# Performance work log

Hardware: AMD Instinct MI355X
Metric: run time of the kernel (lower is better)

## Reference

```python
import jax, jax.numpy as jnp
import numpy as np

EMBED = 1024
HEADS = 16
HEAD_DIM = EMBED // HEADS
B, L = 4, 2048


def setup_inputs() -> dict:
    key = jax.random.key(0)
    ks = jax.random.split(key, 10)
    s = 1.0 / np.sqrt(EMBED)
    x = jax.random.normal(ks[0], (B, L, EMBED), dtype=jnp.float32)
    mask = jax.random.randint(ks[1], (B, 1, L, L), 0, 2, dtype=jnp.int32)
    Wq = jax.random.normal(ks[2], (EMBED, EMBED), dtype=jnp.float32) * s
    Wk = jax.random.normal(ks[3], (EMBED, EMBED), dtype=jnp.float32) * s
    Wv = jax.random.normal(ks[4], (EMBED, EMBED), dtype=jnp.float32) * s
    Wo = jax.random.normal(ks[5], (EMBED, EMBED), dtype=jnp.float32) * s
    bq = jnp.zeros((EMBED,), jnp.float32)
    bk = jnp.zeros((EMBED,), jnp.float32)
    bv = jnp.zeros((EMBED,), jnp.float32)
    bo = jnp.zeros((EMBED,), jnp.float32)
    return {"x": x, "mask": mask, "Wq": Wq, "bq": bq, "Wk": Wk, "bk": bk,
            "Wv": Wv, "bv": bv, "Wo": Wo, "bo": bo}


def reference(x, mask, Wq, bq, Wk, bk, Wv, bv, Wo, bo):
    n, l, _ = x.shape
    q = (x @ Wq + bq).reshape(n, l, HEADS, HEAD_DIM)
    k = (x @ Wk + bk).reshape(n, l, HEADS, HEAD_DIM)
    v = (x @ Wv + bv).reshape(n, l, HEADS, HEAD_DIM)
    # [n, h, q, k] scores
    energy = jnp.einsum('nqhd,nkhd->nhqk', q, k)
    energy = jnp.where(mask == 0, jnp.float32(-1e20), energy)
    attn = jax.nn.softmax(energy / jnp.sqrt(jnp.float32(HEAD_DIM)), axis=-1)
    out = jnp.einsum('nhqk,nkhd->nqhd', attn, v).reshape(n, l, EMBED)
    return out @ Wo + bo
```

## Files before the change

kernel.cpp:

```cpp
#include <hip/hip_runtime.h>
#include <hip/hip_bf16.h>

#define EMBED 1024
#define HEADS 16
#define HDIM 64
#define BATCH 4
#define SEQ 2048
#define ROWS (BATCH * SEQ)
#define LOG2E 1.4426950408889634f

typedef __attribute__((ext_vector_type(8))) short bf16x8;
typedef __attribute__((ext_vector_type(4))) float f32x4;

#define MFMA16(a, b, c) __builtin_amdgcn_mfma_f32_16x16x32_bf16(a, b, c, 0, 0, 0)

__device__ __forceinline__ unsigned short f2bf(float f) {
    union { float f; unsigned int u; } x; x.f = f;
    unsigned int r = x.u + 0x7fffu + ((x.u >> 16) & 1u);
    return (unsigned short)(r >> 16);
}

__device__ __forceinline__ unsigned int pkbf(float a, float b) {
#if __has_builtin(__builtin_amdgcn_cvt_pk_bf16_f32)
    auto v = __builtin_amdgcn_cvt_pk_bf16_f32(a, b);
    unsigned int u; __builtin_memcpy(&u, &v, 4); return u;
#else
    union { __hip_bfloat162 h; unsigned int u; } c;
    c.h = __float22bfloat162_rn(make_float2(a, b)); return c.u;
#endif
}

__device__ __forceinline__ void gl2lds(const unsigned short* g, unsigned short* l) {
    __builtin_amdgcn_global_load_lds(
        (const __attribute__((address_space(1))) unsigned int*)g,
        (__attribute__((address_space(3))) unsigned int*)l, 16, 0, 0);
}

#define XBLK 8192
#define MBLK 16384
#define WBLK 4096

__global__ __launch_bounds__(256) void prep_kernel(
    const float* __restrict__ x, const int* __restrict__ mask,
    const float* __restrict__ W0, const float* __restrict__ W1,
    const float* __restrict__ W2, const float* __restrict__ W3,
    unsigned short* __restrict__ Xb, unsigned char* __restrict__ m8,
    unsigned short* __restrict__ Wt)
{
    __shared__ float t[32][33];
    const int bid = blockIdx.x;
    if (bid < XBLK) {
        int i = (bid * 256 + threadIdx.x) * 4;
        float4 v = *(const float4*)(x + i);
        uint2 o; o.x = pkbf(v.x, v.y); o.y = pkbf(v.z, v.w);
        *(uint2*)(Xb + i) = o;
    } else if (bid < XBLK + MBLK) {
        int i = ((bid - XBLK) * 256 + threadIdx.x) * 4;
        int4 v = *(const int4*)(mask + i);
        uchar4 o;
        o.x = v.x ? 0xFF : 0; o.y = v.y ? 0xFF : 0;
        o.z = v.z ? 0xFF : 0; o.w = v.w ? 0xFF : 0;
        *(uchar4*)(m8 + i) = o;
    } else {
        int f = bid - XBLK - MBLK;
        int z = f >> 10, rem = f & 1023;
        const float* W = (z == 0) ? W0 : (z == 1) ? W1 : (z == 2) ? W2 : W3;
        unsigned short* o = Wt + (size_t)z * EMBED * EMBED;
        int tx = threadIdx.x & 31, ty = threadIdx.x >> 5;
        int bx = (rem & 31) * 32, by = (rem >> 5) * 32;
#pragma unroll
        for (int r = 0; r < 32; r += 8)
            t[ty + r][tx] = W[(size_t)(by + ty + r) * EMBED + bx + tx];
        __syncthreads();
#pragma unroll
        for (int r = 0; r < 32; r += 8)
            o[(size_t)(bx + ty + r) * EMBED + by + tx] = f2bf(t[tx][ty + r]);
    }
}

__device__ __forceinline__ void gemm_bf16_body(
    const unsigned short* __restrict__ A, const unsigned short* __restrict__ Bt,
    const float* __restrict__ bias,
    float* __restrict__ outF, unsigned short* __restrict__ outB, float scale,
    int vmode)
{
    __shared__ unsigned short As[128][64];
    __shared__ unsigned short Bs[128][64];
    const int tid = threadIdx.x;
    const int lane = tid & 63, wid = tid >> 6;
    const int ln = lane & 15, lg = lane >> 4;
    const int wy = wid >> 1, wx = wid & 1;
    const int m0 = blockIdx.y * 128, n0 = blockIdx.x * 128;
    const int r0 = wid * 32 + (lane >> 3);
    const int scol = (((lane & 7) ^ ((lane >> 3) & 7)) << 3);
    const unsigned short* Ap = A + (size_t)(m0 + r0) * EMBED + scol;
    const unsigned short* Bp = Bt + (size_t)(n0 + r0) * EMBED + scol;
    unsigned short* lA = &As[wid * 32][0];
    unsigned short* lB = &Bs[wid * 32][0];

    f32x4 acc[4][4];
#pragma unroll
    for (int i = 0; i < 4; i++)
#pragma unroll
        for (int j = 0; j < 4; j++) acc[i][j] = (f32x4){0.f, 0.f, 0.f, 0.f};

    for (int k0 = 0; k0 < EMBED; k0 += 64) {
        __syncthreads();
#pragma unroll
        for (int is = 0; is < 4; is++) {
            gl2lds(Ap + k0 + (size_t)(is * 8) * EMBED, lA + is * 8 * 64);
            gl2lds(Bp + k0 + (size_t)(is * 8) * EMBED, lB + is * 8 * 64);
        }
        __syncthreads();
        bf16x8 af[2][4], bfr[2][4];
#pragma unroll
        for (int s = 0; s < 2; s++) {
#pragma unroll
            for (int mi = 0; mi < 4; mi++)
                af[s][mi] = *(const bf16x8*)
                    &As[wy * 64 + mi * 16 + ln][(((lg + 4 * s) ^ (ln & 7)) << 3)];
#pragma unroll
            for (int nj = 0; nj < 4; nj++)
                bfr[s][nj] = *(const bf16x8*)
                    &Bs[wx * 64 + nj * 16 + ln][(((lg + 4 * s) ^ (ln & 7)) << 3)];
        }
#pragma unroll
        for (int s = 0; s < 2; s++)
#pragma unroll
            for (int mi = 0; mi < 4; mi++)
#pragma unroll
                for (int nj = 0; nj < 4; nj++)
                    acc[mi][nj] = MFMA16(af[s][mi], bfr[s][nj], acc[mi][nj]);
    }

#pragma unroll
    for (int mi = 0; mi < 4; mi++) {
#pragma unroll
        for (int nj = 0; nj < 4; nj++) {
            int row = m0 + wy * 64 + mi * 16 + lg * 4;
            int col = n0 + wx * 64 + nj * 16 + ln;
            float bv = bias[col];
            if (vmode) {
                int bb = row >> 11, s = row & (SEQ - 1);
                int hh = col >> 6, dd = col & 63;
                unsigned short* dst = outB +
                    ((size_t)((bb * HEADS + hh) * HDIM + dd)) * SEQ + s;
                uint2 pw;
                pw.x = pkbf(acc[mi][nj][0] + bv, acc[mi][nj][1] + bv);
                pw.y = pkbf(acc[mi][nj][2] + bv, acc[mi][nj][3] + bv);
                *(uint2*)dst = pw;
            } else {
#pragma unroll
                for (int r = 0; r < 4; r++) {
                    float v = (acc[mi][nj][r] + bv) * scale;
                    if (outF) outF[(size_t)(row + r) * EMBED + col] = v;
                    else      outB[(size_t)(row + r) * EMBED + col] = f2bf(v);
                }
            }
        }
    }
}

__global__ __launch_bounds__(256) void qkv_gemm_kernel(
    const unsigned short* __restrict__ Xb, const unsigned short* __restrict__ Wt,
    const float* __restrict__ bq, const float* __restrict__ bk,
    const float* __restrict__ bv,
    unsigned short* __restrict__ Qb, unsigned short* __restrict__ Kb,
    unsigned short* __restrict__ Vt)
{
    int z = blockIdx.z;
    const unsigned short* Bt = Wt + (size_t)z * EMBED * EMBED;
    const float* bias = (z == 0) ? bq : (z == 1) ? bk : bv;
    unsigned short* out = (z == 0) ? Qb : (z == 1) ? Kb : Vt;
    float scale = (z == 0) ? 0.125f * LOG2E : 1.0f;
    gemm_bf16_body(Xb, Bt, bias, nullptr, out, scale, z == 2);
}

__global__ __launch_bounds__(256) void out_gemm_kernel(
    const unsigned short* __restrict__ Ob, const unsigned short* __restrict__ Wto,
    const float* __restrict__ bo, float* __restrict__ out)
{
    gemm_bf16_body(Ob, Wto, bo, out, nullptr, 1.0f, 0);
}

__global__ __launch_bounds__(256) void attn_mfma_kernel(
    const unsigned short* __restrict__ Qb, const unsigned short* __restrict__ Kb,
    const unsigned short* __restrict__ Vt, const unsigned char* __restrict__ mask8,
    unsigned short* __restrict__ Ob)
{
    __shared__ unsigned short Ks[64][64];
    __shared__ unsigned short Vs[64][64];
    __shared__ unsigned short Ps[4][32][64];
    const int tid = threadIdx.x;
    const int lane = tid & 63, wid = tid >> 6;
    const int ln = lane & 15, lg = lane >> 4;
    const int b = blockIdx.z, h = blockIdx.y;
    const int q0 = blockIdx.x * 128 + wid * 32;

    bf16x8 qf[2][2];
#pragma unroll
    for (int mi = 0; mi < 2; mi++)
#pragma unroll
        for (int ks = 0; ks < 2; ks++)
            qf[mi][ks] = *(const bf16x8*)(Qb +
                (size_t)(b * SEQ + q0 + mi * 16 + ln) * EMBED + h * HDIM + ks * 32 + lg * 8);

    bf16x8 ones;
#pragma unroll
    for (int i = 0; i < 8; i++) ones[i] = (short)0x3F80;

    f32x4 o[2][4];
#pragma unroll
    for (int mi = 0; mi < 2; mi++)
#pragma unroll
        for (int dj = 0; dj < 4; dj++) o[mi][dj] = (f32x4){0.f, 0.f, 0.f, 0.f};
    f32x4 lacc[2] = {(f32x4){0.f, 0.f, 0.f, 0.f}, (f32x4){0.f, 0.f, 0.f, 0.f}};

    const int srow = tid >> 3;
    const int scolKV = (((tid & 7) ^ ((tid >> 3) & 7)) << 3);
    const unsigned short* Kp = Kb + (size_t)(b * SEQ + srow) * EMBED + h * HDIM + scolKV;
    const unsigned short* Vp = Vt + (size_t)((b * HEADS + h) * HDIM + srow) * SEQ + scolKV;
    unsigned short* lK = &Ks[srow & ~7][0];
    unsigned short* lV = &Vs[srow & ~7][0];

    const unsigned char* mq0 = mask8 + (size_t)b * SEQ * SEQ + (size_t)(q0 + ln) * SEQ;
    const unsigned char* mq1 = mq0 + (size_t)16 * SEQ;

    const int swk = ((lg ^ (ln & 7)) << 3);

    int pwr[4], prd[2];
#pragma unroll
    for (int nj = 0; nj < 4; nj++)
        pwr[nj] = (((2 * nj + (lg >> 1)) ^ (ln & 7)) << 3) + ((lg & 1) << 2);
#pragma unroll
    for (int ks = 0; ks < 2; ks++)
        prd[ks] = ((4 * ks + lg) ^ (ln & 7)) << 3;
    unsigned short* ps0 = &Ps[wid][ln][0];
    unsigned short* ps1 = &Ps[wid][16 + ln][0];

    for (int kt = 0; kt < SEQ; kt += 64) {
        unsigned int mw[2][4];
#pragma unroll
        for (int mi = 0; mi < 2; mi++) {
            const unsigned char* mq = (mi ? mq1 : mq0) + kt;
#pragma unroll
            for (int nj = 0; nj < 4; nj++)
                mw[mi][nj] = *(const unsigned int*)(mq + nj * 16 + lg * 4);
        }

        __syncthreads();
        gl2lds(Kp + (size_t)kt * EMBED, lK);
        gl2lds(Kp + (size_t)(kt + 32) * EMBED, lK + 32 * 64);
        gl2lds(Vp + kt, lV);
        gl2lds(Vp + (size_t)32 * SEQ + kt, lV + 32 * 64);
        __syncthreads();

        f32x4 S[2][4];
#pragma unroll
        for (int nj = 0; nj < 4; nj++) {
            bf16x8 k0 = *(const bf16x8*)&Ks[nj * 16 + ln][swk];
            bf16x8 k1 = *(const bf16x8*)&Ks[nj * 16 + ln][swk ^ 32];
#pragma unroll
            for (int mi = 0; mi < 2; mi++) {
                f32x4 t2 = (f32x4){0.f, 0.f, 0.f, 0.f};
                t2 = MFMA16(k0, qf[mi][0], t2);
                t2 = MFMA16(k1, qf[mi][1], t2);
                S[mi][nj] = t2;
            }
        }

#pragma unroll
        for (int mi = 0; mi < 2; mi++) {
            unsigned short* psb = mi ? ps1 : ps0;
#pragma unroll
            for (int nj = 0; nj < 4; nj++) {
                float p0 = __builtin_amdgcn_exp2f(S[mi][nj][0]);
                float p1 = __builtin_amdgcn_exp2f(S[mi][nj][1]);
                float p2 = __builtin_amdgcn_exp2f(S[mi][nj][2]);
                float p3 = __builtin_amdgcn_exp2f(S[mi][nj][3]);
                unsigned int m = mw[mi][nj];
                unsigned int d0 = __builtin_amdgcn_perm(0u, m, 0x01010000u);
                unsigned int d1 = __builtin_amdgcn_perm(0u, m, 0x03030202u);
                uint2 pw;
                pw.x = pkbf(p0, p1) & d0;
                pw.y = pkbf(p2, p3) & d1;
                *(uint2*)(psb + pwr[nj]) = pw;
            }
        }

#pragma unroll
        for (int ks = 0; ks < 2; ks++) {
            bf16x8 p0 = *(const bf16x8*)(ps0 + prd[ks]);
            bf16x8 p1 = *(const bf16x8*)(ps1 + prd[ks]);
            lacc[0] = MFMA16(p0, ones, lacc[0]);
            lacc[1] = MFMA16(p1, ones, lacc[1]);
#pragma unroll
            for (int dj = 0; dj < 4; dj++) {
                bf16x8 vf = *(const bf16x8*)&Vs[dj * 16 + ln][swk ^ (ks << 5)];
                o[0][dj] = MFMA16(p0, vf, o[0][dj]);
                o[1][dj] = MFMA16(p1, vf, o[1][dj]);
            }
        }
    }

#pragma unroll
    for (int mi = 0; mi < 2; mi++) {
        float l0 = 1.0f / lacc[mi][0];
        float l1 = 1.0f / lacc[mi][1];
        float l2 = 1.0f / lacc[mi][2];
        float l3 = 1.0f / lacc[mi][3];
#pragma unroll
        for (int dj = 0; dj < 4; dj++) {
            unsigned short* op = Ob + (size_t)(b * SEQ + q0 + mi * 16 + lg * 4) * EMBED
                                    + h * HDIM + dj * 16 + ln;
            op[0]         = f2bf(o[mi][dj][0] * l0);
            op[EMBED]     = f2bf(o[mi][dj][1] * l1);
            op[2 * EMBED] = f2bf(o[mi][dj][2] * l2);
            op[3 * EMBED] = f2bf(o[mi][dj][3] * l3);
        }
    }
}

extern "C" void kernel_launch(void* const* d_in, const int* in_sizes, int n_in,
                              void* d_out, int out_size, void* d_ws, size_t ws_size,
                              hipStream_t stream)
{
    const float* x  = (const float*)d_in[0];
    const int* mask = (const int*)d_in[1];
    const float* Wq = (const float*)d_in[2];
    const float* bq = (const float*)d_in[3];
    const float* Wk = (const float*)d_in[4];
    const float* bk = (const float*)d_in[5];
    const float* Wv = (const float*)d_in[6];
    const float* bv = (const float*)d_in[7];
    const float* Wo = (const float*)d_in[8];
    const float* bo = (const float*)d_in[9];
    float* outp = (float*)d_out;

    char* ws = (char*)d_ws;
    unsigned short* Wt = (unsigned short*)(ws);
    unsigned char*  m8 = (unsigned char*)(ws + ((size_t)8 << 20));
    unsigned short* Xb = (unsigned short*)(ws + ((size_t)24 << 20));
    unsigned short* Ob = Xb;
    unsigned short* Qb = (unsigned short*)(ws + ((size_t)40 << 20));
    unsigned short* Kb = (unsigned short*)(ws + ((size_t)56 << 20));
    unsigned short* Vt = (unsigned short*)(ws + ((size_t)72 << 20));

    prep_kernel<<<XBLK + MBLK + WBLK, 256, 0, stream>>>(
        x, mask, Wq, Wk, Wv, Wo, Xb, m8, Wt);
    qkv_gemm_kernel<<<dim3(EMBED / 128, ROWS / 128, 3), 256, 0, stream>>>(
        Xb, Wt, bq, bk, bv, Qb, Kb, Vt);
    attn_mfma_kernel<<<dim3(SEQ / 128, HEADS, BATCH), 256, 0, stream>>>(
        Qb, Kb, Vt, m8, Ob);
    out_gemm_kernel<<<dim3(EMBED / 128, ROWS / 128), 256, 0, stream>>>(
        Ob, Wt + (size_t)3 * EMBED * EMBED, bo, outp);
}
```

Measured before the change: 403.7 us.

## Prefetch next K/V tile into registers during attention compute

Replaces the synchronous per-iteration global-to-LDS copy of K/V tiles with a register prefetch of the next tile, issued before the current tile's MFMA work and written to LDS afterwards. This is meant to hide global load latency behind the QK and PV matrix math. It also raises wave priority around the MFMA sections and sets a minimum-blocks hint in the launch bounds, which may constrain registers and cause spills given the extra prefetch registers.

```diff
diff --git a/kernel.cpp b/kernel.cpp
--- a/kernel.cpp
+++ b/kernel.cpp
@@ -183,7 +183,7 @@
     gemm_bf16_body(Ob, Wto, bo, out, nullptr, 1.0f, 0);
 }
 
-__global__ __launch_bounds__(256) void attn_mfma_kernel(
+__global__ __launch_bounds__(256, 4) void attn_mfma_kernel(
     const unsigned short* __restrict__ Qb, const unsigned short* __restrict__ Kb,
     const unsigned short* __restrict__ Vt, const unsigned char* __restrict__ mask8,
     unsigned short* __restrict__ Ob)
@@ -223,6 +223,14 @@
     unsigned short* lK = &Ks[srow & ~7][0];
     unsigned short* lV = &Vs[srow & ~7][0];
 
+    gl2lds(Kp, lK);
+    gl2lds(Kp + (size_t)32 * EMBED, lK + 32 * 64);
+    gl2lds(Vp, lV);
+    gl2lds(Vp + (size_t)32 * SEQ, lV + 32 * 64);
+
+    unsigned short* wK = lK + lane * 8;
+    unsigned short* wV = lV + lane * 8;
+
     const unsigned char* mq0 = mask8 + (size_t)b * SEQ * SEQ + (size_t)(q0 + ln) * SEQ;
     const unsigned char* mq1 = mq0 + (size_t)16 * SEQ;
 
@@ -238,6 +246,8 @@
     unsigned short* ps0 = &Ps[wid][ln][0];
     unsigned short* ps1 = &Ps[wid][16 + ln][0];
 
+    __syncthreads();
+
     for (int kt = 0; kt < SEQ; kt += 64) {
         unsigned int mw[2][4];
 #pragma unroll
@@ -248,14 +258,17 @@
                 mw[mi][nj] = *(const unsigned int*)(mq + nj * 16 + lg * 4);
         }
 
-        __syncthreads();
-        gl2lds(Kp + (size_t)kt * EMBED, lK);
-        gl2lds(Kp + (size_t)(kt + 32) * EMBED, lK + 32 * 64);
-        gl2lds(Vp + kt, lV);
-        gl2lds(Vp + (size_t)32 * SEQ + kt, lV + 32 * 64);
-        __syncthreads();
+        uint4 nk0, nk1, nv0, nv1;
+        const int ktn = kt + 64;
+        if (ktn < SEQ) {
+            nk0 = *(const uint4*)(Kp + (size_t)ktn * EMBED);
+            nk1 = *(const uint4*)(Kp + (size_t)(ktn + 32) * EMBED);
+            nv0 = *(const uint4*)(Vp + ktn);
+            nv1 = *(const uint4*)(Vp + (size_t)32 * SEQ + ktn);
+        }
 
         f32x4 S[2][4];
+        __builtin_amdgcn_s_setprio(1);
 #pragma unroll
         for (int nj = 0; nj < 4; nj++) {
             bf16x8 k0 = *(const bf16x8*)&Ks[nj * 16 + ln][swk];
@@ -268,6 +281,7 @@
                 S[mi][nj] = t2;
             }
         }
+        __builtin_amdgcn_s_setprio(0);
 
 #pragma unroll
         for (int mi = 0; mi < 2; mi++) {
@@ -288,6 +302,7 @@
             }
         }
 
+        __builtin_amdgcn_s_setprio(1);
 #pragma unroll
         for (int ks = 0; ks < 2; ks++) {
             bf16x8 p0 = *(const bf16x8*)(ps0 + prd[ks]);
@@ -300,6 +315,16 @@
                 o[0][dj] = MFMA16(p0, vf, o[0][dj]);
                 o[1][dj] = MFMA16(p1, vf, o[1][dj]);
             }
+        }
+        __builtin_amdgcn_s_setprio(0);
+
+        if (ktn < SEQ) {
+            __syncthreads();
+            *(uint4*)wK = nk0;
+            *(uint4*)(wK + 32 * 64) = nk1;
+            *(uint4*)wV = nv0;
+            *(uint4*)(wV + 32 * 64) = nv1;
+            __syncthreads();
         }
     }
 
```

Result: slower. 463.2 us (+14.7%).

## Double-buffer K/V tiles with 32-key steps in attention kernel

Applied to the files above, without the earlier changes.

Shrinks the attention key tile from 64 to 32 and double-buffers the K and V tiles in LDS. The next tile's global-to-LDS load is issued before computing on the current one, so each iteration needs one barrier instead of two. MFMA sections are wrapped with s_setprio to favour matrix issue. The price is twice as many loop iterations and barriers, plus new swizzle indexing for the narrower V and P tiles.

```diff
diff --git a/kernel.cpp b/kernel.cpp
--- a/kernel.cpp
+++ b/kernel.cpp
@@ -188,9 +188,9 @@
     const unsigned short* __restrict__ Vt, const unsigned char* __restrict__ mask8,
     unsigned short* __restrict__ Ob)
 {
-    __shared__ unsigned short Ks[64][64];
-    __shared__ unsigned short Vs[64][64];
-    __shared__ unsigned short Ps[4][32][64];
+    __shared__ unsigned short Ks[2][32][64];
+    __shared__ unsigned short Vs[2][64][32];
+    __shared__ unsigned short Ps[4][32][32];
     const int tid = threadIdx.x;
     const int lane = tid & 63, wid = tid >> 6;
     const int ln = lane & 15, lg = lane >> 4;
@@ -217,49 +217,56 @@
     f32x4 lacc[2] = {(f32x4){0.f, 0.f, 0.f, 0.f}, (f32x4){0.f, 0.f, 0.f, 0.f}};
 
     const int srow = tid >> 3;
-    const int scolKV = (((tid & 7) ^ ((tid >> 3) & 7)) << 3);
-    const unsigned short* Kp = Kb + (size_t)(b * SEQ + srow) * EMBED + h * HDIM + scolKV;
-    const unsigned short* Vp = Vt + (size_t)((b * HEADS + h) * HDIM + srow) * SEQ + scolKV;
-    unsigned short* lK = &Ks[srow & ~7][0];
-    unsigned short* lV = &Vs[srow & ~7][0];
+    const int scolK = (((tid & 7) ^ ((tid >> 3) & 7)) << 3);
+    const int vrow = tid >> 2;
+    const int scolV = (((tid & 3) ^ ((tid >> 2) & 3)) << 3);
+    const unsigned short* Kp = Kb + (size_t)(b * SEQ + srow) * EMBED + h * HDIM + scolK;
+    const unsigned short* Vp = Vt + (size_t)((b * HEADS + h) * HDIM + vrow) * SEQ + scolV;
+
+    gl2lds(Kp, &Ks[0][wid * 8][0]);
+    gl2lds(Vp, &Vs[0][wid * 16][0]);
 
     const unsigned char* mq0 = mask8 + (size_t)b * SEQ * SEQ + (size_t)(q0 + ln) * SEQ;
     const unsigned char* mq1 = mq0 + (size_t)16 * SEQ;
 
     const int swk = ((lg ^ (ln & 7)) << 3);
-
-    int pwr[4], prd[2];
-#pragma unroll
-    for (int nj = 0; nj < 4; nj++)
-        pwr[nj] = (((2 * nj + (lg >> 1)) ^ (ln & 7)) << 3) + ((lg & 1) << 2);
-#pragma unroll
-    for (int ks = 0; ks < 2; ks++)
-        prd[ks] = ((4 * ks + lg) ^ (ln & 7)) << 3;
+    const int vswk = ((lg ^ (ln & 3)) << 3);
+
+    int pwr[2];
+#pragma unroll
+    for (int nj = 0; nj < 2; nj++)
+        pwr[nj] = (((2 * nj + (lg >> 1)) ^ (ln & 3)) << 3) + ((lg & 1) << 2);
+    const int prd = ((lg ^ (ln & 3)) << 3);
     unsigned short* ps0 = &Ps[wid][ln][0];
     unsigned short* ps1 = &Ps[wid][16 + ln][0];
 
-    for (int kt = 0; kt < SEQ; kt += 64) {
-        unsigned int mw[2][4];
+    __syncthreads();
+
+    for (int kt = 0; kt < SEQ; kt += 32) {
+        const int cur = (kt >> 5) & 1;
+
+        unsigned int mw[2][2];
 #pragma unroll
         for (int mi = 0; mi < 2; mi++) {
             const unsigned char* mq = (mi ? mq1 : mq0) + kt;
 #pragma unroll
-            for (int nj = 0; nj < 4; nj++)
+            for (int nj = 0; nj < 2; nj++)
                 mw[mi][nj] = *(const unsigned int*)(mq + nj * 16 + lg * 4);
         }
-
-        __syncthreads();
-        gl2lds(Kp + (size_t)kt * EMBED, lK);
-        gl2lds(Kp + (size_t)(kt + 32) * EMBED, lK + 32 * 64);
-        gl2lds(Vp + kt, lV);
-        gl2lds(Vp + (size_t)32 * SEQ + kt, lV + 32 * 64);
-        __syncthreads();
-
-        f32x4 S[2][4];
-#pragma unroll
-        for (int nj = 0; nj < 4; nj++) {
-            bf16x8 k0 = *(const bf16x8*)&Ks[nj * 16 + ln][swk];
-            bf16x8 k1 = *(const bf16x8*)&Ks[nj * 16 + ln][swk ^ 32];
+        __builtin_amdgcn_sched_barrier(0);
+
+        if (kt + 32 < SEQ) {
+            gl2lds(Kp + (size_t)(kt + 32) * EMBED, &Ks[cur ^ 1][wid * 8][0]);
+            gl2lds(Vp + (kt + 32), &Vs[cur ^ 1][wid * 16][0]);
+        }
+        __builtin_amdgcn_sched_barrier(0);
+
+        f32x4 S[2][2];
+        __builtin_amdgcn_s_setprio(1);
+#pragma unroll
+        for (int nj = 0; nj < 2; nj++) {
+            bf16x8 k0 = *(const bf16x8*)&Ks[cur][nj * 16 + ln][swk];
+            bf16x8 k1 = *(const bf16x8*)&Ks[cur][nj * 16 + ln][swk ^ 32];
 #pragma unroll
             for (int mi = 0; mi < 2; mi++) {
                 f32x4 t2 = (f32x4){0.f, 0.f, 0.f, 0.f};
@@ -268,12 +275,13 @@
                 S[mi][nj] = t2;
             }
         }
+        __builtin_amdgcn_s_setprio(0);
 
 #pragma unroll
         for (int mi = 0; mi < 2; mi++) {
             unsigned short* psb = mi ? ps1 : ps0;
 #pragma unroll
-            for (int nj = 0; nj < 4; nj++) {
+            for (int nj = 0; nj < 2; nj++) {
                 float p0 = __builtin_amdgcn_exp2f(S[mi][nj][0]);
                 float p1 = __builtin_amdgcn_exp2f(S[mi][nj][1]);
                 float p2 = __builtin_amdgcn_exp2f(S[mi][nj][2]);
@@ -288,19 +296,22 @@
             }
         }
 
-#pragma unroll
-        for (int ks = 0; ks < 2; ks++) {
-            bf16x8 p0 = *(const bf16x8*)(ps0 + prd[ks]);
-            bf16x8 p1 = *(const bf16x8*)(ps1 + prd[ks]);
+        __builtin_amdgcn_s_setprio(1);
+        {
+            bf16x8 p0 = *(const bf16x8*)(ps0 + prd);
+            bf16x8 p1 = *(const bf16x8*)(ps1 + prd);
             lacc[0] = MFMA16(p0, ones, lacc[0]);
             lacc[1] = MFMA16(p1, ones, lacc[1]);
 #pragma unroll
             for (int dj = 0; dj < 4; dj++) {
-                bf16x8 vf = *(const bf16x8*)&Vs[dj * 16 + ln][swk ^ (ks << 5)];
+                bf16x8 vf = *(const bf16x8*)&Vs[cur][dj * 16 + ln][vswk];
                 o[0][dj] = MFMA16(p0, vf, o[0][dj]);
                 o[1][dj] = MFMA16(p1, vf, o[1][dj]);
             }
         }
+        __builtin_amdgcn_s_setprio(0);
+
+        __syncthreads();
     }
 
 #pragma unroll
```

New measurement: 442.0 us. 9.5% more time.

## Keep softmax probabilities in registers and permute V reads to match MFMA layout

Applied to the files above, without the earlier changes.

Removes the per-wave LDS staging buffer for the probability tile. The exp2 and mask results now go straight into MFMA A-operand registers, and the V fragment loads are split into two 4-element reads so their K ordering matches the register layout of P. This avoids an LDS write/read round trip and frees shared memory, at the cost of twice as many narrower V loads. s_setprio hints are also added around the MFMA phases.

```diff
diff --git a/kernel.cpp b/kernel.cpp
--- a/kernel.cpp
+++ b/kernel.cpp
@@ -10,6 +10,7 @@
 #define LOG2E 1.4426950408889634f
 
 typedef __attribute__((ext_vector_type(8))) short bf16x8;
+typedef __attribute__((ext_vector_type(4))) short bf16x4;
 typedef __attribute__((ext_vector_type(4))) float f32x4;
 
 #define MFMA16(a, b, c) __builtin_amdgcn_mfma_f32_16x16x32_bf16(a, b, c, 0, 0, 0)
@@ -190,7 +191,6 @@
 {
     __shared__ unsigned short Ks[64][64];
     __shared__ unsigned short Vs[64][64];
-    __shared__ unsigned short Ps[4][32][64];
     const int tid = threadIdx.x;
     const int lane = tid & 63, wid = tid >> 6;
     const int ln = lane & 15, lg = lane >> 4;
@@ -228,15 +228,14 @@
 
     const int swk = ((lg ^ (ln & 7)) << 3);
 
-    int pwr[4], prd[2];
-#pragma unroll
-    for (int nj = 0; nj < 4; nj++)
-        pwr[nj] = (((2 * nj + (lg >> 1)) ^ (ln & 7)) << 3) + ((lg & 1) << 2);
-#pragma unroll
-    for (int ks = 0; ks < 2; ks++)
-        prd[ks] = ((4 * ks + lg) ^ (ln & 7)) << 3;
-    unsigned short* ps0 = &Ps[wid][ln][0];
-    unsigned short* ps1 = &Ps[wid][16 + ln][0];
+    int vc0[2], vc1[2];
+#pragma unroll
+    for (int ks = 0; ks < 2; ks++) {
+        vc0[ks] = (((4 * ks + (lg >> 1)) ^ (ln & 7)) << 3) + ((lg & 1) << 2);
+        vc1[ks] = (((4 * ks + 2 + (lg >> 1)) ^ (ln & 7)) << 3) + ((lg & 1) << 2);
+    }
+
+    union U8 { bf16x8 v; unsigned int w[4]; };
 
     for (int kt = 0; kt < SEQ; kt += 64) {
         unsigned int mw[2][4];
@@ -256,6 +255,7 @@
         __syncthreads();
 
         f32x4 S[2][4];
+        __builtin_amdgcn_s_setprio(1);
 #pragma unroll
         for (int nj = 0; nj < 4; nj++) {
             bf16x8 k0 = *(const bf16x8*)&Ks[nj * 16 + ln][swk];
@@ -268,39 +268,45 @@
                 S[mi][nj] = t2;
             }
         }
-
-#pragma unroll
-        for (int mi = 0; mi < 2; mi++) {
-            unsigned short* psb = mi ? ps1 : ps0;
-#pragma unroll
-            for (int nj = 0; nj < 4; nj++) {
-                float p0 = __builtin_amdgcn_exp2f(S[mi][nj][0]);
-                float p1 = __builtin_amdgcn_exp2f(S[mi][nj][1]);
-                float p2 = __builtin_amdgcn_exp2f(S[mi][nj][2]);
-                float p3 = __builtin_amdgcn_exp2f(S[mi][nj][3]);
-                unsigned int m = mw[mi][nj];
-                unsigned int d0 = __builtin_amdgcn_perm(0u, m, 0x01010000u);
-                unsigned int d1 = __builtin_amdgcn_perm(0u, m, 0x03030202u);
-                uint2 pw;
-                pw.x = pkbf(p0, p1) & d0;
-                pw.y = pkbf(p2, p3) & d1;
-                *(uint2*)(psb + pwr[nj]) = pw;
-            }
-        }
-
+        __builtin_amdgcn_s_setprio(0);
+
+        U8 pf[2][2];
+#pragma unroll
+        for (int mi = 0; mi < 2; mi++)
+#pragma unroll
+            for (int ks = 0; ks < 2; ks++)
+#pragma unroll
+                for (int hf = 0; hf < 2; hf++) {
+                    const int nj = 2 * ks + hf;
+                    float p0 = __builtin_amdgcn_exp2f(S[mi][nj][0]);
+                    float p1 = __builtin_amdgcn_exp2f(S[mi][nj][1]);
+                    float p2 = __builtin_amdgcn_exp2f(S[mi][nj][2]);
+                    float p3 = __builtin_amdgcn_exp2f(S[mi][nj][3]);
+                    unsigned int m = mw[mi][nj];
+                    unsigned int d0 = __builtin_amdgcn_perm(0u, m, 0x01010000u);
+                    unsigned int d1 = __builtin_amdgcn_perm(0u, m, 0x03030202u);
+                    pf[mi][ks].w[2 * hf]     = pkbf(p0, p1) & d0;
+                    pf[mi][ks].w[2 * hf + 1] = pkbf(p2, p3) & d1;
+                }
+
+        __builtin_amdgcn_s_setprio(1);
 #pragma unroll
         for (int ks = 0; ks < 2; ks++) {
-            bf16x8 p0 = *(const bf16x8*)(ps0 + prd[ks]);
-            bf16x8 p1 = *(const bf16x8*)(ps1 + prd[ks]);
+            bf16x8 p0 = pf[0][ks].v;
+            bf16x8 p1 = pf[1][ks].v;
             lacc[0] = MFMA16(p0, ones, lacc[0]);
             lacc[1] = MFMA16(p1, ones, lacc[1]);
 #pragma unroll
             for (int dj = 0; dj < 4; dj++) {
-                bf16x8 vf = *(const bf16x8*)&Vs[dj * 16 + ln][swk ^ (ks << 5)];
+                const unsigned short* vrow = &Vs[dj * 16 + ln][0];
+                bf16x4 vlo = *(const bf16x4*)(vrow + vc0[ks]);
+                bf16x4 vhi = *(const bf16x4*)(vrow + vc1[ks]);
+                bf16x8 vf = __builtin_shufflevector(vlo, vhi, 0, 1, 2, 3, 4, 5, 6, 7);
                 o[0][dj] = MFMA16(p0, vf, o[0][dj]);
                 o[1][dj] = MFMA16(p1, vf, o[1][dj]);
             }
         }
+        __builtin_amdgcn_s_setprio(0);
     }
 
 #pragma unroll
```

New measurement: 413.2 us. +2.4%, slower.
